# Performance work log

Hardware: AMD Instinct MI355X
Metric: run time of the kernel (lower is better)

The kernel has to match this reference:

```python
import jax, jax.numpy as jnp
import numpy as np

B, TO, C, T = 16, 8, 64, 1024


def setup_inputs() -> dict:
    key = jax.random.key(0)
    kx, kq, kk, kv, ko = jax.random.split(key, 5)
    s = 0.1
    return {
        "x": jax.random.normal(kx, (B, TO, C, T), dtype=jnp.float32),
        "Wq": jax.random.normal(kq, (C, C), dtype=jnp.float32) * s,
        "Wk": jax.random.normal(kk, (C, C), dtype=jnp.float32) * s,
        "Wv": jax.random.normal(kv, (C, C), dtype=jnp.float32) * s,
        "Wo": jax.random.normal(ko, (C, C), dtype=jnp.float32) * s,
        "scale": jnp.float32(1.0 / np.sqrt(C)),
    }


def reference(x, Wq, Wk, Wv, Wo, scale):
    b, to, c, t = x.shape
    xr = x.reshape(b * to, c, t)            # [N, C, T]
    # 1x1 conv1d (no bias) == channel-mixing matmul with weight [out_c, in_c]
    q = jnp.einsum('oc,bct->bot', Wq, xr)
    k = jnp.einsum('oc,bct->bot', Wk, xr)
    v = jnp.einsum('oc,bct->bot', Wv, xr)
    # attention over the time axis: scores [N, T, T]
    scores = jnp.einsum('bct,bcs->bts', q, k) * scale
    w = jax.nn.softmax(scores, axis=-1)
    out = jnp.einsum('bts,bcs->bct', w, v)  # [N, C, T]
    out = jnp.einsum('oc,bct->bot', Wo, out)
    out = out + xr
    return out.reshape(b, to, c, t)
```

## Files before the change

### kernel.cpp

```cpp
#include <hip/hip_runtime.h>
#include <hip/hip_bf16.h>

typedef __hip_bfloat16 bf16;
typedef __attribute__((ext_vector_type(8))) short short8;
typedef __attribute__((ext_vector_type(4))) short short4v;
typedef __attribute__((ext_vector_type(4))) float f32x4;
typedef __attribute__((ext_vector_type(4))) unsigned uint4v;

#define NB 128
#define CC 64
#define TT 1024

#if __has_builtin(__builtin_amdgcn_exp2f)
#define EXP2(x) __builtin_amdgcn_exp2f(x)
#else
#define EXP2(x) exp2f(x)
#endif

__device__ __forceinline__ unsigned rnd_u(float f) {
  return __builtin_bit_cast(unsigned, f) + 0x8000u;
}
__device__ __forceinline__ unsigned packbf2(unsigned uhi, unsigned ulo) {
  return __builtin_amdgcn_perm(uhi, ulo, 0x07060302);
}
__device__ __forceinline__ short4v pack4(float a, float b, float c, float d) {
  unsigned pd[2] = { packbf2(rnd_u(b), rnd_u(a)), packbf2(rnd_u(d), rnd_u(c)) };
  return *(const short4v*)pd;
}

__device__ __forceinline__ f32x4 mfma32(short8 a, short8 b, f32x4 c) {
  return __builtin_amdgcn_mfma_f32_16x16x32_bf16(a, b, c, 0, 0, 0);
}

__global__ __launch_bounds__(256) void wprep(
    const float* __restrict__ Wq, const float* __restrict__ Wk,
    const float* __restrict__ Wv, const float* __restrict__ Wo,
    const float* __restrict__ scale_p, bf16* __restrict__ wmw)
{
  const int g = blockIdx.x * 256 + threadIdx.x;
  float acc = 0.f;
  if (g < 4096) {
    const int a = g >> 6, b = g & 63;
    #pragma unroll 8
    for (int c = 0; c < 64; c++) acc += Wk[c * 64 + a] * Wq[c * 64 + b];
    acc *= (*scale_p) * 1.44269504089f;
    wmw[g] = __float2bfloat16(acc);
  } else {
    const int ii = g - 4096;
    const int o = ii >> 6, cp = ii & 63;
    const int u = cp >> 5, q4 = (cp >> 3) & 3, j = cp & 7;
    const int a = (2 * u + (j >> 2)) * 16 + q4 * 4 + (j & 3);
    #pragma unroll 8
    for (int c = 0; c < 64; c++) acc += Wo[o * 64 + c] * Wv[c * 64 + a];
    wmw[g] = __float2bfloat16(acc);
  }
}

__global__ __launch_bounds__(256, 4) void attn_fused(
    const bf16* __restrict__ wm, const bf16* __restrict__ w2,
    const float* __restrict__ x, float* __restrict__ out)
{
  __shared__ float obuf[64 * 132];
  short* xq = (short*)obuf;
  short* ks = (short*)obuf;
  short* vs = ks + 64 * 72;

  const int bid = blockIdx.x;
  const int n   = bid & 127;
  const int qt0 = (bid >> 7) * 128;
  const int tid = threadIdx.x;
  const int w   = tid >> 6;
  const int il  = tid & 15;
  const int q4  = (tid & 63) >> 4;
  const size_t nbase = (size_t)n * (CC * TT);

  const int ts  = tid & 31;
  const int cg  = tid >> 5;
  const int krow = ts * 2;
  const int sp0 = ((ts >> 1) & 3) * 16 + (ts >> 3) * 4 + (ts & 1) * 2;

  #pragma unroll
  for (int half = 0; half < 2; half++) {
    float2 xr[8];
    #pragma unroll
    for (int j = 0; j < 8; j++)
      xr[j] = *(const float2*)&x[nbase + (size_t)(cg * 8 + j) * TT + qt0 + half * 64 + ts * 2];
    #pragma unroll
    for (int e = 0; e < 2; e++) {
      unsigned kd[4];
      #pragma unroll
      for (int d = 0; d < 4; d++) {
        float lo = e ? xr[2 * d].y     : xr[2 * d].x;
        float hi = e ? xr[2 * d + 1].y : xr[2 * d + 1].x;
        kd[d] = packbf2(rnd_u(hi), rnd_u(lo));
      }
      *(uint4v*)&xq[(half * 64 + krow + e) * 72 + cg * 8] = *(const uint4v*)kd;
    }
  }
  __syncthreads();

  f32x4 yacc[4][2];
  #pragma unroll
  for (int at = 0; at < 4; at++)
    #pragma unroll
    for (int mt = 0; mt < 2; mt++) yacc[at][mt] = (f32x4){0.f, 0.f, 0.f, 0.f};
  #pragma unroll
  for (int kk = 0; kk < 2; kk++) {
    short8 xb0 = *(const short8*)&xq[(w * 32 + il) * 72 + kk * 32 + q4 * 8];
    short8 xb1 = *(const short8*)&xq[(w * 32 + 16 + il) * 72 + kk * 32 + q4 * 8];
    #pragma unroll
    for (int at = 0; at < 4; at++) {
      short8 ma = *(const short8*)&wm[(at * 16 + il) * 64 + kk * 32 + q4 * 8];
      yacc[at][0] = mfma32(ma, xb0, yacc[at][0]);
      yacc[at][1] = mfma32(ma, xb1, yacc[at][1]);
    }
  }
  __syncthreads();
  #pragma unroll
  for (int at = 0; at < 4; at++)
    #pragma unroll
    for (int mt = 0; mt < 2; mt++)
      *(short4v*)&xq[(w * 32 + mt * 16 + il) * 72 + at * 16 + q4 * 4] =
          pack4(yacc[at][mt][0], yacc[at][mt][1], yacc[at][mt][2], yacc[at][mt][3]);
  __syncthreads();
  short8 yb[2][2];
  #pragma unroll
  for (int mt = 0; mt < 2; mt++)
    #pragma unroll
    for (int kk = 0; kk < 2; kk++)
      yb[mt][kk] = *(const short8*)&xq[(w * 32 + mt * 16 + il) * 72 + kk * 32 + q4 * 8];

  const short8 ones8 = { 0x3F80, 0x3F80, 0x3F80, 0x3F80,
                         0x3F80, 0x3F80, 0x3F80, 0x3F80 };

  f32x4 oaccT[2][4];
  f32x4 lacc[2];
  #pragma unroll
  for (int mt = 0; mt < 2; mt++) {
    lacc[mt] = (f32x4){0.f, 0.f, 0.f, 0.f};
    #pragma unroll
    for (int ct = 0; ct < 4; ct++) oaccT[mt][ct] = (f32x4){0.f, 0.f, 0.f, 0.f};
  }

  float2 xr[8];
  #pragma unroll
  for (int j = 0; j < 8; j++)
    xr[j] = *(const float2*)&x[nbase + (size_t)(cg * 8 + j) * TT + ts * 2];

  #pragma unroll 1
  for (int st = 0; st < 16; st++) {
    __syncthreads();
    #pragma unroll
    for (int e = 0; e < 2; e++) {
      unsigned kd[4];
      #pragma unroll
      for (int d = 0; d < 4; d++) {
        float lo = e ? xr[2 * d].y     : xr[2 * d].x;
        float hi = e ? xr[2 * d + 1].y : xr[2 * d + 1].x;
        kd[d] = packbf2(rnd_u(hi), rnd_u(lo));
      }
      *(uint4v*)&ks[(krow + e) * 72 + cg * 8] = *(const uint4v*)kd;
    }
    #pragma unroll
    for (int j = 0; j < 8; j++)
      *(unsigned*)&vs[(cg * 8 + j) * 72 + sp0] = packbf2(rnd_u(xr[j].y), rnd_u(xr[j].x));
    if (st < 15) {
      const int s1 = (st + 1) * 64;
      #pragma unroll
      for (int j = 0; j < 8; j++)
        xr[j] = *(const float2*)&x[nbase + (size_t)(cg * 8 + j) * TT + s1 + ts * 2];
    }
    __syncthreads();

    __builtin_amdgcn_s_setprio(1);

    uint4v pq[2][2];
    #pragma unroll
    for (int st2 = 0; st2 < 4; st2++) {
      short8 ka0 = *(const short8*)&ks[(st2 * 16 + il) * 72 + q4 * 8];
      short8 ka1 = *(const short8*)&ks[(st2 * 16 + il) * 72 + 32 + q4 * 8];
      #pragma unroll
      for (int mt = 0; mt < 2; mt++) {
        f32x4 sT = (f32x4){0.f, 0.f, 0.f, 0.f};
        sT = mfma32(ka0, yb[mt][0], sT);
        sT = mfma32(ka1, yb[mt][1], sT);
        float p0 = EXP2(sT[0]), p1 = EXP2(sT[1]), p2 = EXP2(sT[2]), p3 = EXP2(sT[3]);
        pq[mt][st2 >> 1][(st2 & 1) * 2]     = packbf2(rnd_u(p1), rnd_u(p0));
        pq[mt][st2 >> 1][(st2 & 1) * 2 + 1] = packbf2(rnd_u(p3), rnd_u(p2));
      }
    }
    short8 pb[2][2];
    #pragma unroll
    for (int mt = 0; mt < 2; mt++)
      #pragma unroll
      for (int u = 0; u < 2; u++) {
        pb[mt][u] = __builtin_bit_cast(short8, pq[mt][u]);
        lacc[mt] = mfma32(ones8, pb[mt][u], lacc[mt]);
      }

    #pragma unroll
    for (int ct = 0; ct < 4; ct++) {
      short8 h0 = *(const short8*)&vs[(ct * 16 + il) * 72 + q4 * 16];
      short8 h1 = *(const short8*)&vs[(ct * 16 + il) * 72 + q4 * 16 + 8];
      #pragma unroll
      for (int mt = 0; mt < 2; mt++) {
        oaccT[mt][ct] = mfma32(h0, pb[mt][0], oaccT[mt][ct]);
        oaccT[mt][ct] = mfma32(h1, pb[mt][1], oaccT[mt][ct]);
      }
    }

    __builtin_amdgcn_s_setprio(0);
  }

  float linv[2];
  #pragma unroll
  for (int mt = 0; mt < 2; mt++) linv[mt] = 1.f / lacc[mt][0];

  uint4v obq[2][2];
  #pragma unroll
  for (int mt = 0; mt < 2; mt++)
    #pragma unroll
    for (int ct = 0; ct < 4; ct++) {
      float a = oaccT[mt][ct][0] * linv[mt], b = oaccT[mt][ct][1] * linv[mt];
      float c = oaccT[mt][ct][2] * linv[mt], d = oaccT[mt][ct][3] * linv[mt];
      obq[mt][ct >> 1][(ct & 1) * 2]     = packbf2(rnd_u(b), rnd_u(a));
      obq[mt][ct >> 1][(ct & 1) * 2 + 1] = packbf2(rnd_u(d), rnd_u(c));
    }
  short8 ob8[2][2];
  #pragma unroll
  for (int mt = 0; mt < 2; mt++)
    #pragma unroll
    for (int u = 0; u < 2; u++)
      ob8[mt][u] = __builtin_bit_cast(short8, obq[mt][u]);

  __syncthreads();

  #pragma unroll
  for (int ot = 0; ot < 4; ot++) {
    short8 wa0 = *(const short8*)&w2[(ot * 16 + il) * 64 + q4 * 8];
    short8 wa1 = *(const short8*)&w2[(ot * 16 + il) * 64 + 32 + q4 * 8];
    #pragma unroll
    for (int mt = 0; mt < 2; mt++) {
      f32x4 res = (f32x4){0.f, 0.f, 0.f, 0.f};
      res = mfma32(wa0, ob8[mt][0], res);
      res = mfma32(wa1, ob8[mt][1], res);
      #pragma unroll
      for (int r = 0; r < 4; r++)
        obuf[(ot * 16 + q4 * 4 + r) * 132 + w * 32 + mt * 16 + il] = res[r];
    }
  }
  __syncthreads();

  const int orow = tid >> 3;
  const int ocb  = (tid & 7) * 4;
  #pragma unroll
  for (int half = 0; half < 2; half++) {
    const int row = orow + half * 32;
    #pragma unroll
    for (int k = 0; k < 4; k++) {
      const int col = ocb + k * 32;
      float4 val = *(const float4*)&obuf[row * 132 + col];
      const size_t idx = nbase + (size_t)row * TT + qt0 + col;
      float4 xv = *(const float4*)&x[idx];
      val.x += xv.x; val.y += xv.y; val.z += xv.z; val.w += xv.w;
      *(float4*)&out[idx] = val;
    }
  }
}

extern "C" void kernel_launch(void* const* d_in, const int* in_sizes, int n_in,
                              void* d_out, int out_size, void* d_ws, size_t ws_size,
                              hipStream_t stream) {
  const float* x     = (const float*)d_in[0];
  const float* Wq    = (const float*)d_in[1];
  const float* Wk    = (const float*)d_in[2];
  const float* Wv    = (const float*)d_in[3];
  const float* Wo    = (const float*)d_in[4];
  const float* scale = (const float*)d_in[5];
  float* out = (float*)d_out;

  bf16* wmw = (bf16*)d_ws;

  wprep<<<32, 256, 0, stream>>>(Wq, Wk, Wv, Wo, scale, wmw);
  attn_fused<<<1024, 256, 0, stream>>>(wmw, wmw + 4096, x, out);
}
```

Before: 134.8 us.

## Halve query tile per block to 64 and double grid with higher occupancy

Each block now handles 64 query positions instead of 128, so every wave processes one 16-row query tile instead of two. The grid doubles to 2048 blocks, shared memory shrinks to 18 KB, and launch bounds ask for 8 blocks per CU, which cuts register pressure and raises occupancy. In exchange, each K/V tile staged in LDS is reused by half as many queries, so the global reads of x for K/V and the conversion work are doubled.

```diff
diff --git a/kernel.cpp b/kernel.cpp
--- a/kernel.cpp
+++ b/kernel.cpp
@@ -56,18 +56,18 @@
   }
 }
 
-__global__ __launch_bounds__(256, 4) void attn_fused(
+__global__ __launch_bounds__(256, 8) void attn_fused(
     const bf16* __restrict__ wm, const bf16* __restrict__ w2,
     const float* __restrict__ x, float* __restrict__ out)
 {
-  __shared__ float obuf[64 * 132];
+  __shared__ float obuf[4608];
   short* xq = (short*)obuf;
   short* ks = (short*)obuf;
-  short* vs = ks + 64 * 72;
+  short* vs = ks + 4608;
 
   const int bid = blockIdx.x;
   const int n   = bid & 127;
-  const int qt0 = (bid >> 7) * 128;
+  const int qt0 = (bid >> 7) * 64;
   const int tid = threadIdx.x;
   const int w   = tid >> 6;
   const int il  = tid & 15;
@@ -79,68 +79,55 @@
   const int krow = ts * 2;
   const int sp0 = ((ts >> 1) & 3) * 16 + (ts >> 3) * 4 + (ts & 1) * 2;
 
-  #pragma unroll
-  for (int half = 0; half < 2; half++) {
-    float2 xr[8];
+  {
+    float2 xr0[8];
     #pragma unroll
     for (int j = 0; j < 8; j++)
-      xr[j] = *(const float2*)&x[nbase + (size_t)(cg * 8 + j) * TT + qt0 + half * 64 + ts * 2];
+      xr0[j] = *(const float2*)&x[nbase + (size_t)(cg * 8 + j) * TT + qt0 + ts * 2];
     #pragma unroll
     for (int e = 0; e < 2; e++) {
       unsigned kd[4];
       #pragma unroll
       for (int d = 0; d < 4; d++) {
-        float lo = e ? xr[2 * d].y     : xr[2 * d].x;
-        float hi = e ? xr[2 * d + 1].y : xr[2 * d + 1].x;
+        float lo = e ? xr0[2 * d].y     : xr0[2 * d].x;
+        float hi = e ? xr0[2 * d + 1].y : xr0[2 * d + 1].x;
         kd[d] = packbf2(rnd_u(hi), rnd_u(lo));
       }
-      *(uint4v*)&xq[(half * 64 + krow + e) * 72 + cg * 8] = *(const uint4v*)kd;
-    }
-  }
-  __syncthreads();
-
-  f32x4 yacc[4][2];
-  #pragma unroll
-  for (int at = 0; at < 4; at++)
-    #pragma unroll
-    for (int mt = 0; mt < 2; mt++) yacc[at][mt] = (f32x4){0.f, 0.f, 0.f, 0.f};
+      *(uint4v*)&xq[(krow + e) * 72 + cg * 8] = *(const uint4v*)kd;
+    }
+  }
+  __syncthreads();
+
+  f32x4 yacc[4];
+  #pragma unroll
+  for (int at = 0; at < 4; at++) yacc[at] = (f32x4){0.f, 0.f, 0.f, 0.f};
   #pragma unroll
   for (int kk = 0; kk < 2; kk++) {
-    short8 xb0 = *(const short8*)&xq[(w * 32 + il) * 72 + kk * 32 + q4 * 8];
-    short8 xb1 = *(const short8*)&xq[(w * 32 + 16 + il) * 72 + kk * 32 + q4 * 8];
+    short8 xb = *(const short8*)&xq[(w * 16 + il) * 72 + kk * 32 + q4 * 8];
     #pragma unroll
     for (int at = 0; at < 4; at++) {
       short8 ma = *(const short8*)&wm[(at * 16 + il) * 64 + kk * 32 + q4 * 8];
-      yacc[at][0] = mfma32(ma, xb0, yacc[at][0]);
-      yacc[at][1] = mfma32(ma, xb1, yacc[at][1]);
+      yacc[at] = mfma32(ma, xb, yacc[at]);
     }
   }
   __syncthreads();
   #pragma unroll
   for (int at = 0; at < 4; at++)
-    #pragma unroll
-    for (int mt = 0; mt < 2; mt++)
-      *(short4v*)&xq[(w * 32 + mt * 16 + il) * 72 + at * 16 + q4 * 4] =
-          pack4(yacc[at][mt][0], yacc[at][mt][1], yacc[at][mt][2], yacc[at][mt][3]);
-  __syncthreads();
-  short8 yb[2][2];
-  #pragma unroll
-  for (int mt = 0; mt < 2; mt++)
-    #pragma unroll
-    for (int kk = 0; kk < 2; kk++)
-      yb[mt][kk] = *(const short8*)&xq[(w * 32 + mt * 16 + il) * 72 + kk * 32 + q4 * 8];
+    *(short4v*)&xq[(w * 16 + il) * 72 + at * 16 + q4 * 4] =
+        pack4(yacc[at][0], yacc[at][1], yacc[at][2], yacc[at][3]);
+  __syncthreads();
+  short8 yb[2];
+  #pragma unroll
+  for (int kk = 0; kk < 2; kk++)
+    yb[kk] = *(const short8*)&xq[(w * 16 + il) * 72 + kk * 32 + q4 * 8];
 
   const short8 ones8 = { 0x3F80, 0x3F80, 0x3F80, 0x3F80,
                          0x3F80, 0x3F80, 0x3F80, 0x3F80 };
 
-  f32x4 oaccT[2][4];
-  f32x4 lacc[2];
-  #pragma unroll
-  for (int mt = 0; mt < 2; mt++) {
-    lacc[mt] = (f32x4){0.f, 0.f, 0.f, 0.f};
-    #pragma unroll
-    for (int ct = 0; ct < 4; ct++) oaccT[mt][ct] = (f32x4){0.f, 0.f, 0.f, 0.f};
-  }
+  f32x4 oaccT[4];
+  f32x4 lacc = (f32x4){0.f, 0.f, 0.f, 0.f};
+  #pragma unroll
+  for (int ct = 0; ct < 4; ct++) oaccT[ct] = (f32x4){0.f, 0.f, 0.f, 0.f};
 
   float2 xr[8];
   #pragma unroll
@@ -174,64 +161,50 @@
 
     __builtin_amdgcn_s_setprio(1);
 
-    uint4v pq[2][2];
+    uint4v pq[2];
     #pragma unroll
     for (int st2 = 0; st2 < 4; st2++) {
       short8 ka0 = *(const short8*)&ks[(st2 * 16 + il) * 72 + q4 * 8];
       short8 ka1 = *(const short8*)&ks[(st2 * 16 + il) * 72 + 32 + q4 * 8];
-      #pragma unroll
-      for (int mt = 0; mt < 2; mt++) {
-        f32x4 sT = (f32x4){0.f, 0.f, 0.f, 0.f};
-        sT = mfma32(ka0, yb[mt][0], sT);
-        sT = mfma32(ka1, yb[mt][1], sT);
-        float p0 = EXP2(sT[0]), p1 = EXP2(sT[1]), p2 = EXP2(sT[2]), p3 = EXP2(sT[3]);
-        pq[mt][st2 >> 1][(st2 & 1) * 2]     = packbf2(rnd_u(p1), rnd_u(p0));
-        pq[mt][st2 >> 1][(st2 & 1) * 2 + 1] = packbf2(rnd_u(p3), rnd_u(p2));
-      }
-    }
-    short8 pb[2][2];
-    #pragma unroll
-    for (int mt = 0; mt < 2; mt++)
-      #pragma unroll
-      for (int u = 0; u < 2; u++) {
-        pb[mt][u] = __builtin_bit_cast(short8, pq[mt][u]);
-        lacc[mt] = mfma32(ones8, pb[mt][u], lacc[mt]);
-      }
+      f32x4 sT = (f32x4){0.f, 0.f, 0.f, 0.f};
+      sT = mfma32(ka0, yb[0], sT);
+      sT = mfma32(ka1, yb[1], sT);
+      float p0 = EXP2(sT[0]), p1 = EXP2(sT[1]), p2 = EXP2(sT[2]), p3 = EXP2(sT[3]);
+      pq[st2 >> 1][(st2 & 1) * 2]     = packbf2(rnd_u(p1), rnd_u(p0));
+      pq[st2 >> 1][(st2 & 1) * 2 + 1] = packbf2(rnd_u(p3), rnd_u(p2));
+    }
+    short8 pb[2];
+    #pragma unroll
+    for (int u = 0; u < 2; u++) {
+      pb[u] = __builtin_bit_cast(short8, pq[u]);
+      lacc = mfma32(ones8, pb[u], lacc);
+    }
 
     #pragma unroll
     for (int ct = 0; ct < 4; ct++) {
       short8 h0 = *(const short8*)&vs[(ct * 16 + il) * 72 + q4 * 16];
       short8 h1 = *(const short8*)&vs[(ct * 16 + il) * 72 + q4 * 16 + 8];
-      #pragma unroll
-      for (int mt = 0; mt < 2; mt++) {
-        oaccT[mt][ct] = mfma32(h0, pb[mt][0], oaccT[mt][ct]);
-        oaccT[mt][ct] = mfma32(h1, pb[mt][1], oaccT[mt][ct]);
-      }
+      oaccT[ct] = mfma32(h0, pb[0], oaccT[ct]);
+      oaccT[ct] = mfma32(h1, pb[1], oaccT[ct]);
     }
 
     __builtin_amdgcn_s_setprio(0);
   }
 
-  float linv[2];
-  #pragma unroll
-  for (int mt = 0; mt < 2; mt++) linv[mt] = 1.f / lacc[mt][0];
-
-  uint4v obq[2][2];
-  #pragma unroll
-  for (int mt = 0; mt < 2; mt++)
-    #pragma unroll
-    for (int ct = 0; ct < 4; ct++) {
-      float a = oaccT[mt][ct][0] * linv[mt], b = oaccT[mt][ct][1] * linv[mt];
-      float c = oaccT[mt][ct][2] * linv[mt], d = oaccT[mt][ct][3] * linv[mt];
-      obq[mt][ct >> 1][(ct & 1) * 2]     = packbf2(rnd_u(b), rnd_u(a));
-      obq[mt][ct >> 1][(ct & 1) * 2 + 1] = packbf2(rnd_u(d), rnd_u(c));
-    }
-  short8 ob8[2][2];
-  #pragma unroll
-  for (int mt = 0; mt < 2; mt++)
-    #pragma unroll
-    for (int u = 0; u < 2; u++)
-      ob8[mt][u] = __builtin_bit_cast(short8, obq[mt][u]);
+  const float linv = 1.f / lacc[0];
+
+  uint4v obq[2];
+  #pragma unroll
+  for (int ct = 0; ct < 4; ct++) {
+    float a = oaccT[ct][0] * linv, b = oaccT[ct][1] * linv;
+    float c = oaccT[ct][2] * linv, d = oaccT[ct][3] * linv;
+    obq[ct >> 1][(ct & 1) * 2]     = packbf2(rnd_u(b), rnd_u(a));
+    obq[ct >> 1][(ct & 1) * 2 + 1] = packbf2(rnd_u(d), rnd_u(c));
+  }
+  short8 ob8[2];
+  #pragma unroll
+  for (int u = 0; u < 2; u++)
+    ob8[u] = __builtin_bit_cast(short8, obq[u]);
 
   __syncthreads();
 
@@ -239,15 +212,12 @@
   for (int ot = 0; ot < 4; ot++) {
     short8 wa0 = *(const short8*)&w2[(ot * 16 + il) * 64 + q4 * 8];
     short8 wa1 = *(const short8*)&w2[(ot * 16 + il) * 64 + 32 + q4 * 8];
-    #pragma unroll
-    for (int mt = 0; mt < 2; mt++) {
-      f32x4 res = (f32x4){0.f, 0.f, 0.f, 0.f};
-      res = mfma32(wa0, ob8[mt][0], res);
-      res = mfma32(wa1, ob8[mt][1], res);
-      #pragma unroll
-      for (int r = 0; r < 4; r++)
-        obuf[(ot * 16 + q4 * 4 + r) * 132 + w * 32 + mt * 16 + il] = res[r];
-    }
+    f32x4 res = (f32x4){0.f, 0.f, 0.f, 0.f};
+    res = mfma32(wa0, ob8[0], res);
+    res = mfma32(wa1, ob8[1], res);
+    #pragma unroll
+    for (int r = 0; r < 4; r++)
+      obuf[(ot * 16 + q4 * 4 + r) * 68 + w * 16 + il] = res[r];
   }
   __syncthreads();
 
@@ -257,9 +227,9 @@
   for (int half = 0; half < 2; half++) {
     const int row = orow + half * 32;
     #pragma unroll
-    for (int k = 0; k < 4; k++) {
+    for (int k = 0; k < 2; k++) {
       const int col = ocb + k * 32;
-      float4 val = *(const float4*)&obuf[row * 132 + col];
+      float4 val = *(const float4*)&obuf[row * 68 + col];
       const size_t idx = nbase + (size_t)row * TT + qt0 + col;
       float4 xv = *(const float4*)&x[idx];
       val.x += xv.x; val.y += xv.y; val.z += xv.z; val.w += xv.w;
@@ -282,5 +252,5 @@
   bf16* wmw = (bf16*)d_ws;
 
   wprep<<<32, 256, 0, stream>>>(Wq, Wk, Wv, Wo, scale, wmw);
-  attn_fused<<<1024, 256, 0, stream>>>(wmw, wmw + 4096, x, out);
-}
+  attn_fused<<<2048, 256, 0, stream>>>(wmw, wmw + 4096, x, out);
+}
```

Result: slower. 192.8 us (+43.0%).
